# Kernel tuning notes

Hardware: AMD Instinct MI355X
Metric: run time of the kernel (lower is better)

Reference implementation:

```python
import jax, jax.numpy as jnp
import numpy as np

EPS = 1e-5

def conv1x1(x, w, b):
    # x: [B,C,H,W], w: [O,C], b: [O]
    return jnp.einsum('bchw,oc->bohw', x, w) + b[None, :, None, None]

def bn_eval(x, w, b, m, v):
    inv = w / jnp.sqrt(v + EPS)
    return (x - m[None, :, None, None]) * inv[None, :, None, None] + b[None, :, None, None]

def setup_inputs() -> dict:
    key = jax.random.key(0)
    ks = jax.random.split(key, 32)
    B, Fg, Fl, Fi, H, W = 4, 128, 128, 64, 64, 64
    d = {}
    d['g'] = jax.random.normal(ks[0], (B, Fg, H, W), jnp.float32)
    d['x'] = jax.random.normal(ks[1], (B, Fl, H, W), jnp.float32)
    d['wg_w'] = jax.random.normal(ks[2], (Fi, Fg), jnp.float32) * 0.1
    d['wg_b'] = jax.random.normal(ks[3], (Fi,), jnp.float32) * 0.1
    d['bng_w'] = jax.random.uniform(ks[4], (Fi,), jnp.float32)
    d['bng_b'] = jax.random.normal(ks[5], (Fi,), jnp.float32) * 0.1
    d['bng_m'] = jax.random.normal(ks[6], (Fi,), jnp.float32) * 0.1
    d['bng_v'] = jax.random.uniform(ks[7], (Fi,), jnp.float32) + 0.5
    d['wx_w'] = jax.random.normal(ks[8], (Fi, Fl), jnp.float32) * 0.1
    d['wx_b'] = jax.random.normal(ks[9], (Fi,), jnp.float32) * 0.1
    d['bnx_w'] = jax.random.uniform(ks[10], (Fi,), jnp.float32)
    d['bnx_b'] = jax.random.normal(ks[11], (Fi,), jnp.float32) * 0.1
    d['bnx_m'] = jax.random.normal(ks[12], (Fi,), jnp.float32) * 0.1
    d['bnx_v'] = jax.random.uniform(ks[13], (Fi,), jnp.float32) + 0.5
    d['q_w'] = jax.random.normal(ks[14], (Fi // 8, Fi), jnp.float32) * 0.1
    d['q_b'] = jax.random.normal(ks[15], (Fi // 8,), jnp.float32) * 0.1
    d['k_w'] = jax.random.normal(ks[16], (Fi // 8, Fi), jnp.float32) * 0.1
    d['k_b'] = jax.random.normal(ks[17], (Fi // 8,), jnp.float32) * 0.1
    d['v_w'] = jax.random.normal(ks[18], (Fi, Fi), jnp.float32) * 0.1
    d['v_b'] = jax.random.normal(ks[19], (Fi,), jnp.float32) * 0.1
    d['sa_gamma'] = jax.random.normal(ks[20], (1,), jnp.float32)
    d['psi_w'] = jax.random.normal(ks[21], (1, Fi), jnp.float32) * 0.1
    d['psi_b'] = jax.random.normal(ks[22], (1,), jnp.float32) * 0.1
    d['bnp_w'] = jax.random.uniform(ks[23], (1,), jnp.float32)
    d['bnp_b'] = jax.random.normal(ks[24], (1,), jnp.float32) * 0.1
    d['bnp_m'] = jax.random.normal(ks[25], (1,), jnp.float32) * 0.1
    d['bnp_v'] = jax.random.uniform(ks[26], (1,), jnp.float32) + 0.5
    return d

def reference(g, x, wg_w, wg_b, bng_w, bng_b, bng_m, bng_v,
              wx_w, wx_b, bnx_w, bnx_b, bnx_m, bnx_v,
              q_w, q_b, k_w, k_b, v_w, v_b, sa_gamma,
              psi_w, psi_b, bnp_w, bnp_b, bnp_m, bnp_v):
    g1 = bn_eval(conv1x1(g, wg_w, wg_b), bng_w, bng_b, bng_m, bng_v)
    x1 = bn_eval(conv1x1(x, wx_w, wx_b), bnx_w, bnx_b, bnx_m, bnx_v)
    c = jax.nn.relu(g1 + x1)  # [B, Fi, H, W]
    B, C, H, W = c.shape
    N = H * W
    q = conv1x1(c, q_w, q_b).reshape(B, -1, N)  # [B, Fi/8, N]
    k = conv1x1(c, k_w, k_b).reshape(B, -1, N)
    v = conv1x1(c, v_w, v_b).reshape(B, C, N)
    energy = jnp.einsum('bcn,bcm->bnm', q, k)    # [B, N, N]
    attn = jax.nn.softmax(energy, axis=-1)
    sa_out = jnp.einsum('bcm,bnm->bcn', v, attn).reshape(B, C, H, W)
    attended = sa_gamma[0] * sa_out + c
    psi = jax.nn.sigmoid(bn_eval(conv1x1(attended, psi_w, psi_b), bnp_w, bnp_b, bnp_m, bnp_v))
    return x * psi
```

## Files before the change

### kernel.cpp

```cpp
#include <hip/hip_runtime.h>
#include <hip/hip_bf16.h>


typedef short bf16x8 __attribute__((ext_vector_type(8)));
typedef unsigned short u16x8 __attribute__((ext_vector_type(8)));
typedef unsigned short u16x4 __attribute__((ext_vector_type(4)));
typedef float f32x4 __attribute__((ext_vector_type(4)));

__device__ __forceinline__ unsigned short f2b16(float f) {
  return __builtin_bit_cast(unsigned short, __float2bfloat16(f));
}
__device__ __forceinline__ float b2f(unsigned short u) {
  return __bfloat162float(__builtin_bit_cast(__hip_bfloat16, u));
}

#define EPSV 1e-5f
#define LOG2E 1.44269504088896340736f

#define C_OFF      0u
#define Q_OFF      (C_OFF + 2097152u)
#define K_OFF      (Q_OFF + 262144u)
#define V_OFF      (K_OFF + 262144u)
#define OPART_OFF  (V_OFF + 2097152u)
#define ML_OFF     (OPART_OFF + 16777216u)

__global__ __launch_bounds__(256) void conv_fused_kernel(
    const float* __restrict__ g, const float* __restrict__ x,
    const float* __restrict__ wg_w, const float* __restrict__ wg_b,
    const float* __restrict__ bng_w, const float* __restrict__ bng_b,
    const float* __restrict__ bng_m, const float* __restrict__ bng_v,
    const float* __restrict__ wx_w, const float* __restrict__ wx_b,
    const float* __restrict__ bnx_w, const float* __restrict__ bnx_b,
    const float* __restrict__ bnx_m, const float* __restrict__ bnx_v,
    const float* __restrict__ q_w, const float* __restrict__ q_b,
    const float* __restrict__ k_w, const float* __restrict__ k_b,
    const float* __restrict__ v_w, const float* __restrict__ v_b,
    unsigned short* __restrict__ cb, unsigned short* __restrict__ Qb,
    unsigned short* __restrict__ Kb, unsigned short* __restrict__ Vb)
{
  __shared__ __attribute__((aligned(16))) unsigned short xt[32][264];
  __shared__ __attribute__((aligned(16))) unsigned short clds[32][72];
  __shared__ __attribute__((aligned(16))) unsigned short vstage[64][36];

  const int t = threadIdx.x;
  const int bid = blockIdx.x;
  const int b = bid >> 7;
  const int n0 = (bid & 127) << 5;

  {
    const int col4 = t & 7;
    const int rowg = t >> 3;
    float4 v[8];
    #pragma unroll
    for (int rr = 0; rr < 8; ++rr) {
      int row = rowg * 8 + rr;
      const float* src = (row < 128)
          ? (g + ((size_t)(b * 128 + row)) * 4096 + n0 + col4 * 4)
          : (x + ((size_t)(b * 128 + (row - 128))) * 4096 + n0 + col4 * 4);
      v[rr] = *(const float4*)src;
    }
    #pragma unroll
    for (int j = 0; j < 4; ++j) {
      u16x8 pk;
      #pragma unroll
      for (int rr = 0; rr < 8; ++rr)
        pk[rr] = f2b16(((const float*)&v[rr])[j]);
      *(u16x8*)(&xt[col4 * 4 + j][rowg * 8]) = pk;
    }
  }

  const int l = t & 63, w = t >> 6;
  const int l15 = l & 15, lg = l >> 4;
  f32x4 zf = {0.f, 0.f, 0.f, 0.f};

  const int orow = w * 16 + l15;
  const float invg = bng_w[orow] * rsqrtf(bng_v[orow] + EPSV);
  const float invx = bnx_w[orow] * rsqrtf(bnx_v[orow] + EPSV);
  bf16x8 afrag[8];
  #pragma unroll
  for (int ks = 0; ks < 8; ++ks) {
    int k = ks * 32 + lg * 8;
    const float* wp;
    float sc;
    if (k < 128) { wp = wg_w + orow * 128 + k;         sc = invg; }
    else         { wp = wx_w + orow * 128 + (k - 128); sc = invx; }
    float4 w0 = *(const float4*)wp;
    float4 w1 = *(const float4*)(wp + 4);
    u16x8 pk;
    pk[0] = f2b16(w0.x * sc); pk[1] = f2b16(w0.y * sc);
    pk[2] = f2b16(w0.z * sc); pk[3] = f2b16(w0.w * sc);
    pk[4] = f2b16(w1.x * sc); pk[5] = f2b16(w1.y * sc);
    pk[6] = f2b16(w1.z * sc); pk[7] = f2b16(w1.w * sc);
    afrag[ks] = __builtin_bit_cast(bf16x8, pk);
  }
  __syncthreads();

  f32x4 acc[2];
  acc[0] = acc[1] = zf;
  #pragma unroll
  for (int ks = 0; ks < 8; ++ks) {
    #pragma unroll
    for (int ns = 0; ns < 2; ++ns) {
      bf16x8 bfv = *(const bf16x8*)(&xt[ns * 16 + l15][ks * 32 + lg * 8]);
      acc[ns] = __builtin_amdgcn_mfma_f32_16x16x32_bf16(afrag[ks], bfv, acc[ns], 0, 0, 0);
    }
  }
  #pragma unroll
  for (int r = 0; r < 4; ++r) {
    int o = w * 16 + lg * 4 + r;
    float ig = bng_w[o] * rsqrtf(bng_v[o] + EPSV);
    float ix = bnx_w[o] * rsqrtf(bnx_v[o] + EPSV);
    float bc = (wg_b[o] - bng_m[o]) * ig + bng_b[o]
             + (wx_b[o] - bnx_m[o]) * ix + bnx_b[o];
    #pragma unroll
    for (int ns = 0; ns < 2; ++ns) {
      float cv = fmaxf(acc[ns][r] + bc, 0.f);
      unsigned short cv16 = f2b16(cv);
      cb[((size_t)(b * 64 + o)) * 4096 + n0 + ns * 16 + l15] = cv16;
      clds[ns * 16 + l15][o] = cv16;
    }
  }
  __syncthreads();

  #pragma unroll
  for (int i = 0; i < 3; ++i) {
    int tau = w + 4 * i;
    if (tau >= 10) break;
    int t5 = tau % 5, ns = tau / 5;
    int wrow = t5 * 16 + l15;
    f32x4 a2 = zf;
    #pragma unroll
    for (int kk = 0; kk < 2; ++kk) {
      int k = kk * 32 + lg * 8;
      const float* wp = (wrow < 8)  ? (q_w + wrow * 64 + k)
                      : (wrow < 16) ? (k_w + (wrow - 8) * 64 + k)
                                    : (v_w + (wrow - 16) * 64 + k);
      float4 w0 = *(const float4*)wp;
      float4 w1 = *(const float4*)(wp + 4);
      u16x8 pk;
      pk[0] = f2b16(w0.x); pk[1] = f2b16(w0.y);
      pk[2] = f2b16(w0.z); pk[3] = f2b16(w0.w);
      pk[4] = f2b16(w1.x); pk[5] = f2b16(w1.y);
      pk[6] = f2b16(w1.z); pk[7] = f2b16(w1.w);
      bf16x8 bfv = *(const bf16x8*)(&clds[ns * 16 + l15][k]);
      a2 = __builtin_amdgcn_mfma_f32_16x16x32_bf16(
          __builtin_bit_cast(bf16x8, pk), bfv, a2, 0, 0, 0);
    }
    int ngl = n0 + ns * 16 + l15;
    if (t5 == 0) {
      u16x4 pk;
      #pragma unroll
      for (int r = 0; r < 4; ++r) {
        int row = lg * 4 + r;
        float val;
        if (row < 8) val = (a2[r] + q_b[row]) * LOG2E;
        else         val = a2[r] + k_b[row - 8];
        pk[r] = f2b16(val);
      }
      if (lg < 2)
        *(u16x4*)(Qb + (((size_t)b << 12) + ngl) * 8 + lg * 4) = pk;
      else
        *(u16x4*)(Kb + (((size_t)b << 12) + ngl) * 8 + (lg - 2) * 4) = pk;
    } else {
      #pragma unroll
      for (int r = 0; r < 4; ++r) {
        int vch = (t5 - 1) * 16 + lg * 4 + r;
        vstage[vch][ns * 16 + l15] = f2b16(a2[r] + v_b[vch]);
      }
    }
  }
  __syncthreads();

  #pragma unroll
  for (int i = 0; i < 2; ++i) {
    int idx = t + 256 * i;
    int row = idx >> 3, seg = idx & 7;
    u16x4 pv = *(const u16x4*)(&vstage[row][seg * 4]);
    *(u16x4*)(Vb + ((size_t)(b * 64 + row)) * 4096 + n0 + seg * 4) = pv;
  }
}

__global__ __launch_bounds__(256) void attn_partial_kernel(
    const unsigned short* __restrict__ Qb, const unsigned short* __restrict__ Kb,
    const unsigned short* __restrict__ Vb,
    unsigned short* __restrict__ Opart, float* __restrict__ ml)
{
  __shared__ __attribute__((aligned(16))) unsigned short klds[64][8];
  __shared__ __attribute__((aligned(16))) unsigned short vlds[64][72];
  __shared__ __attribute__((aligned(16))) unsigned short plds[4][2][16][40];

  const int t = threadIdx.x;
  const int bid = blockIdx.x;
  const int qt = bid & 63;
  const int b = (bid >> 6) & 3;
  const int ci = bid >> 8;
  const int n0 = qt << 6;
  const int l = t & 63, w = t >> 6;
  const int l15 = l & 15, lg = l >> 4;

  bf16x8 qf = {0, 0, 0, 0, 0, 0, 0, 0};
  if (lg == 0)
    qf = *(const bf16x8*)(Qb + (((size_t)b << 12) + n0 + w * 16 + l15) * 8);

  f32x4 zf = {0.f, 0.f, 0.f, 0.f};
  f32x4 O[4];
  O[0] = O[1] = O[2] = O[3] = zf;
  float m_run = -INFINITY;
  float l_run = 0.f;

  const int vrow0 = t >> 3, voff0 = t & 7;
  const unsigned short* Kb_base = Kb + ((size_t)b << 12) * 8;
  const unsigned short* Vb_base = Vb + ((size_t)(b * 64)) * 4096;

  const int m_lo = ci << 9, m_hi = (ci + 1) << 9;

  int4 kreg{}, vreg0{}, vreg1{};
  if (t < 64)
    kreg = *(const int4*)(Kb_base + (size_t)(m_lo + t) * 8);
  vreg0 = *(const int4*)(Vb_base + (size_t)vrow0 * 4096 + m_lo + voff0 * 8);
  vreg1 = *(const int4*)(Vb_base + (size_t)(vrow0 + 32) * 4096 + m_lo + voff0 * 8);

  for (int m0 = m_lo; m0 < m_hi; m0 += 64) {
    if (t < 64) *(int4*)(&klds[t][0]) = kreg;
    *(int4*)(&vlds[vrow0][voff0 * 8]) = vreg0;
    *(int4*)(&vlds[vrow0 + 32][voff0 * 8]) = vreg1;
    __syncthreads();

    if (m0 + 64 < m_hi) {
      if (t < 64)
        kreg = *(const int4*)(Kb_base + (size_t)(m0 + 64 + t) * 8);
      vreg0 = *(const int4*)(Vb_base + (size_t)vrow0 * 4096 + (m0 + 64) + voff0 * 8);
      vreg1 = *(const int4*)(Vb_base + (size_t)(vrow0 + 32) * 4096 + (m0 + 64) + voff0 * 8);
    }

    f32x4 e[4];
    #pragma unroll
    for (int mt = 0; mt < 4; ++mt) {
      bf16x8 kf = *(const bf16x8*)(&klds[mt * 16 + l15][0]);
      e[mt] = __builtin_amdgcn_mfma_f32_16x16x32_bf16(kf, qf, zf, 0, 0, 0);
    }

    float vm = fmaxf(fmaxf(fmaxf(e[0][0], e[0][1]), fmaxf(e[0][2], e[0][3])),
                     fmaxf(fmaxf(e[1][0], e[1][1]), fmaxf(e[1][2], e[1][3])));
    float vm2 = fmaxf(fmaxf(fmaxf(e[2][0], e[2][1]), fmaxf(e[2][2], e[2][3])),
                      fmaxf(fmaxf(e[3][0], e[3][1]), fmaxf(e[3][2], e[3][3])));
    vm = fmaxf(vm, vm2);
    vm = fmaxf(vm, __shfl_xor(vm, 16));
    vm = fmaxf(vm, __shfl_xor(vm, 32));

    bool nosk = __any(vm > m_run + 8.f);
    float nm = nosk ? fmaxf(m_run, vm) : m_run;
    float s = 0.f;
    #pragma unroll
    for (int mt = 0; mt < 4; ++mt) {
      #pragma unroll
      for (int r = 0; r < 4; ++r) {
        float p = __builtin_amdgcn_exp2f(e[mt][r] - nm);
        e[mt][r] = p;
        s += p;
      }
    }
    s += __shfl_xor(s, 16);
    s += __shfl_xor(s, 32);
    if (nosk) {
      float sc = __builtin_amdgcn_exp2f(m_run - nm);
      l_run = l_run * sc + s;
      m_run = nm;
      #pragma unroll
      for (int ct = 0; ct < 4; ++ct)
        #pragma unroll
        for (int r = 0; r < 4; ++r) O[ct][r] *= sc;
    } else {
      l_run += s;
    }

    #pragma unroll
    for (int mt = 0; mt < 4; ++mt) {
      u16x4 pk;
      #pragma unroll
      for (int r = 0; r < 4; ++r) pk[r] = f2b16(e[mt][r]);
      int kk = mt >> 1;
      int lgr = 2 * (mt & 1) + (lg >> 1);
      int j0 = 4 * (lg & 1);
      *(u16x4*)(&plds[w][kk][l15][lgr * 8 + j0]) = pk;
    }

    #pragma unroll
    for (int ct = 0; ct < 4; ++ct) {
      #pragma unroll
      for (int kk = 0; kk < 2; ++kk) {
        bf16x8 pfr = *(const bf16x8*)(&plds[w][kk][l15][lg * 8]);
        bf16x8 vf = *(const bf16x8*)(&vlds[ct * 16 + l15][kk * 32 + lg * 8]);
        O[ct] = __builtin_amdgcn_mfma_f32_16x16x32_bf16(vf, pfr, O[ct], 0, 0, 0);
      }
    }
    __syncthreads();
  }

  const size_t pb = ((size_t)(ci * 4 + b)) << 12;
  const int qg = n0 + w * 16 + l15;
  #pragma unroll
  for (int ct = 0; ct < 4; ++ct) {
    u16x4 pk;
    #pragma unroll
    for (int r = 0; r < 4; ++r) pk[r] = f2b16(O[ct][r]);
    *(u16x4*)(Opart + (pb + qg) * 64 + ct * 16 + lg * 4) = pk;
  }
  if (lg == 0) {
    float2 mv;
    mv.x = m_run; mv.y = l_run;
    *(float2*)(ml + (pb + qg) * 2) = mv;
  }
}

__global__ __launch_bounds__(256) void combine_kernel(
    const unsigned short* __restrict__ Opart, const float* __restrict__ ml,
    const unsigned short* __restrict__ cb, const float* __restrict__ xin,
    const float* __restrict__ psi_w, const float* __restrict__ psi_b,
    const float* __restrict__ bnp_w, const float* __restrict__ bnp_b,
    const float* __restrict__ bnp_m, const float* __restrict__ bnp_v,
    const float* __restrict__ sa_gamma,
    float* __restrict__ out)
{
  __shared__ __attribute__((aligned(16))) unsigned short c_lds[64][20];
  __shared__ __attribute__((aligned(8))) float2 ml_lds[16][8];
  __shared__ float psi_lds[16];

  const int t = threadIdx.x;
  const int bid = blockIdx.x;
  const int b = bid >> 8;
  const int n0 = (bid & 255) << 4;

  {
    int row = t >> 2, seg = t & 3;
    *(u16x4*)(&c_lds[row][seg * 4]) =
        *(const u16x4*)(cb + ((size_t)(b * 64 + row)) * 4096 + n0 + seg * 4);
  }
  if (t < 128) {
    int q = t >> 3, ci = t & 7;
    ml_lds[q][ci] = *(const float2*)(ml + ((((size_t)(ci * 4 + b)) << 12) + n0 + q) * 2);
  }
  __syncthreads();

  const float invp = bnp_w[0] * rsqrtf(bnp_v[0] + EPSV);
  const float psi_c = (psi_b[0] - bnp_m[0]) * invp + bnp_b[0];
  const float gamma = sa_gamma[0];

  const int q = t >> 4, cg = t & 15;
  const int qg = n0 + q;

  float M = -INFINITY;
  #pragma unroll
  for (int ci = 0; ci < 8; ++ci) M = fmaxf(M, ml_lds[q][ci].x);
  float L = 0.f, wgt[8];
  #pragma unroll
  for (int ci = 0; ci < 8; ++ci) {
    wgt[ci] = __builtin_amdgcn_exp2f(ml_lds[q][ci].x - M);
    L += wgt[ci] * ml_lds[q][ci].y;
  }
  float o4[4] = {0.f, 0.f, 0.f, 0.f};
  #pragma unroll
  for (int ci = 0; ci < 8; ++ci) {
    u16x4 p = *(const u16x4*)(Opart + ((((size_t)(ci * 4 + b)) << 12) + qg) * 64 + cg * 4);
    float wv = wgt[ci];
    #pragma unroll
    for (int k = 0; k < 4; ++k) o4[k] += wv * b2f(p[k]);
  }
  const float invL = 1.f / L;
  float ps = 0.f;
  #pragma unroll
  for (int k = 0; k < 4; ++k) {
    int ch = cg * 4 + k;
    ps += (psi_w[ch] * invp) * (gamma * (o4[k] * invL) + b2f(c_lds[ch][q]));
  }
  ps += __shfl_xor(ps, 1);
  ps += __shfl_xor(ps, 2);
  ps += __shfl_xor(ps, 4);
  ps += __shfl_xor(ps, 8);
  if (cg == 0)
    psi_lds[q] = 1.f / (1.f + __expf(-(ps + psi_c)));
  __syncthreads();

  #pragma unroll
  for (int i = 0; i < 2; ++i) {
    int idx = t + 256 * i;
    int f = idx >> 2, c4 = idx & 3;
    size_t off = ((size_t)(b * 128 + f)) * 4096 + n0 + c4 * 4;
    float4 xv = *(const float4*)(xin + off);
    float4 ov;
    ov.x = xv.x * psi_lds[c4 * 4 + 0];
    ov.y = xv.y * psi_lds[c4 * 4 + 1];
    ov.z = xv.z * psi_lds[c4 * 4 + 2];
    ov.w = xv.w * psi_lds[c4 * 4 + 3];
    *(float4*)(out + off) = ov;
  }
}

extern "C" void kernel_launch(void* const* d_in, const int* in_sizes, int n_in,
                              void* d_out, int out_size, void* d_ws, size_t ws_size,
                              hipStream_t stream) {
  (void)in_sizes; (void)n_in; (void)out_size; (void)ws_size;
  const float* g     = (const float*)d_in[0];
  const float* x     = (const float*)d_in[1];
  const float* wg_w  = (const float*)d_in[2];
  const float* wg_b  = (const float*)d_in[3];
  const float* bng_w = (const float*)d_in[4];
  const float* bng_b = (const float*)d_in[5];
  const float* bng_m = (const float*)d_in[6];
  const float* bng_v = (const float*)d_in[7];
  const float* wx_w  = (const float*)d_in[8];
  const float* wx_b  = (const float*)d_in[9];
  const float* bnx_w = (const float*)d_in[10];
  const float* bnx_b = (const float*)d_in[11];
  const float* bnx_m = (const float*)d_in[12];
  const float* bnx_v = (const float*)d_in[13];
  const float* q_w   = (const float*)d_in[14];
  const float* q_b   = (const float*)d_in[15];
  const float* k_w   = (const float*)d_in[16];
  const float* k_b   = (const float*)d_in[17];
  const float* v_w   = (const float*)d_in[18];
  const float* v_b   = (const float*)d_in[19];
  const float* sa_g  = (const float*)d_in[20];
  const float* psi_w = (const float*)d_in[21];
  const float* psi_b = (const float*)d_in[22];
  const float* bnp_w = (const float*)d_in[23];
  const float* bnp_b = (const float*)d_in[24];
  const float* bnp_m = (const float*)d_in[25];
  const float* bnp_v = (const float*)d_in[26];
  float* out = (float*)d_out;

  char* ws = (char*)d_ws;
  unsigned short* cb = (unsigned short*)(ws + C_OFF);
  unsigned short* Qb = (unsigned short*)(ws + Q_OFF);
  unsigned short* Kb = (unsigned short*)(ws + K_OFF);
  unsigned short* Vb = (unsigned short*)(ws + V_OFF);
  unsigned short* Opart = (unsigned short*)(ws + OPART_OFF);
  float* mlb = (float*)(ws + ML_OFF);

  hipLaunchKernelGGL(conv_fused_kernel, dim3(512), dim3(256), 0, stream,
                     g, x, wg_w, wg_b, bng_w, bng_b, bng_m, bng_v,
                     wx_w, wx_b, bnx_w, bnx_b, bnx_m, bnx_v,
                     q_w, q_b, k_w, k_b, v_w, v_b,
                     cb, Qb, Kb, Vb);

  hipLaunchKernelGGL(attn_partial_kernel, dim3(2048), dim3(256), 0, stream,
                     Qb, Kb, Vb, Opart, mlb);

  hipLaunchKernelGGL(combine_kernel, dim3(1024), dim3(256), 0, stream,
                     Opart, mlb, cb, x,
                     psi_w, psi_b, bnp_w, bnp_b, bnp_m, bnp_v, sa_g,
                     out);
}
```

Before: 160.4 us.

## Process two query tiles per attention block to reuse staged K/V tiles

Each attention-partial block now handles 128 queries (two 64-query subtiles) instead of 64, so every K/V tile staged into shared memory feeds twice the MFMA work. The grid is halved to 1024 blocks. This cuts global K/V traffic and per-tile staging and barrier overhead per query. In exchange it raises register pressure (two O accumulators and two running max/sum pairs) and halves the block count, which may hurt occupancy or tail balance on the GPU.

```diff
diff --git a/kernel.cpp b/kernel.cpp
--- a/kernel.cpp
+++ b/kernel.cpp
@@ -191,22 +191,27 @@
 
   const int t = threadIdx.x;
   const int bid = blockIdx.x;
-  const int qt = bid & 63;
-  const int b = (bid >> 6) & 3;
-  const int ci = bid >> 8;
-  const int n0 = qt << 6;
+  const int qp = bid & 31;
+  const int b = (bid >> 5) & 3;
+  const int ci = bid >> 7;
+  const int n0 = qp << 7;
   const int l = t & 63, w = t >> 6;
   const int l15 = l & 15, lg = l >> 4;
 
-  bf16x8 qf = {0, 0, 0, 0, 0, 0, 0, 0};
-  if (lg == 0)
-    qf = *(const bf16x8*)(Qb + (((size_t)b << 12) + n0 + w * 16 + l15) * 8);
+  bf16x8 qf0 = {0, 0, 0, 0, 0, 0, 0, 0};
+  bf16x8 qf1 = {0, 0, 0, 0, 0, 0, 0, 0};
+  if (lg == 0) {
+    qf0 = *(const bf16x8*)(Qb + (((size_t)b << 12) + n0 + w * 16 + l15) * 8);
+    qf1 = *(const bf16x8*)(Qb + (((size_t)b << 12) + n0 + 64 + w * 16 + l15) * 8);
+  }
 
   f32x4 zf = {0.f, 0.f, 0.f, 0.f};
-  f32x4 O[4];
-  O[0] = O[1] = O[2] = O[3] = zf;
-  float m_run = -INFINITY;
-  float l_run = 0.f;
+  f32x4 O[2][4];
+  #pragma unroll
+  for (int qt = 0; qt < 2; ++qt)
+    O[qt][0] = O[qt][1] = O[qt][2] = O[qt][3] = zf;
+  float m_run[2] = {-INFINITY, -INFINITY};
+  float l_run[2] = {0.f, 0.f};
 
   const int vrow0 = t >> 3, voff0 = t & 7;
   const unsigned short* Kb_base = Kb + ((size_t)b << 12) * 8;
@@ -233,83 +238,91 @@
       vreg1 = *(const int4*)(Vb_base + (size_t)(vrow0 + 32) * 4096 + (m0 + 64) + voff0 * 8);
     }
 
-    f32x4 e[4];
-    #pragma unroll
-    for (int mt = 0; mt < 4; ++mt) {
-      bf16x8 kf = *(const bf16x8*)(&klds[mt * 16 + l15][0]);
-      e[mt] = __builtin_amdgcn_mfma_f32_16x16x32_bf16(kf, qf, zf, 0, 0, 0);
-    }
-
-    float vm = fmaxf(fmaxf(fmaxf(e[0][0], e[0][1]), fmaxf(e[0][2], e[0][3])),
-                     fmaxf(fmaxf(e[1][0], e[1][1]), fmaxf(e[1][2], e[1][3])));
-    float vm2 = fmaxf(fmaxf(fmaxf(e[2][0], e[2][1]), fmaxf(e[2][2], e[2][3])),
-                      fmaxf(fmaxf(e[3][0], e[3][1]), fmaxf(e[3][2], e[3][3])));
-    vm = fmaxf(vm, vm2);
-    vm = fmaxf(vm, __shfl_xor(vm, 16));
-    vm = fmaxf(vm, __shfl_xor(vm, 32));
-
-    bool nosk = __any(vm > m_run + 8.f);
-    float nm = nosk ? fmaxf(m_run, vm) : m_run;
-    float s = 0.f;
-    #pragma unroll
-    for (int mt = 0; mt < 4; ++mt) {
-      #pragma unroll
-      for (int r = 0; r < 4; ++r) {
-        float p = __builtin_amdgcn_exp2f(e[mt][r] - nm);
-        e[mt][r] = p;
-        s += p;
-      }
-    }
-    s += __shfl_xor(s, 16);
-    s += __shfl_xor(s, 32);
-    if (nosk) {
-      float sc = __builtin_amdgcn_exp2f(m_run - nm);
-      l_run = l_run * sc + s;
-      m_run = nm;
-      #pragma unroll
-      for (int ct = 0; ct < 4; ++ct)
+    #pragma unroll
+    for (int qt = 0; qt < 2; ++qt) {
+      bf16x8 qf = qt ? qf1 : qf0;
+
+      f32x4 e[4];
+      #pragma unroll
+      for (int mt = 0; mt < 4; ++mt) {
+        bf16x8 kf = *(const bf16x8*)(&klds[mt * 16 + l15][0]);
+        e[mt] = __builtin_amdgcn_mfma_f32_16x16x32_bf16(kf, qf, zf, 0, 0, 0);
+      }
+
+      float vm = fmaxf(fmaxf(fmaxf(e[0][0], e[0][1]), fmaxf(e[0][2], e[0][3])),
+                       fmaxf(fmaxf(e[1][0], e[1][1]), fmaxf(e[1][2], e[1][3])));
+      float vm2 = fmaxf(fmaxf(fmaxf(e[2][0], e[2][1]), fmaxf(e[2][2], e[2][3])),
+                        fmaxf(fmaxf(e[3][0], e[3][1]), fmaxf(e[3][2], e[3][3])));
+      vm = fmaxf(vm, vm2);
+      vm = fmaxf(vm, __shfl_xor(vm, 16));
+      vm = fmaxf(vm, __shfl_xor(vm, 32));
+
+      bool nosk = __any(vm > m_run[qt] + 8.f);
+      float nm = nosk ? fmaxf(m_run[qt], vm) : m_run[qt];
+      float s = 0.f;
+      #pragma unroll
+      for (int mt = 0; mt < 4; ++mt) {
         #pragma unroll
-        for (int r = 0; r < 4; ++r) O[ct][r] *= sc;
-    } else {
-      l_run += s;
-    }
-
-    #pragma unroll
-    for (int mt = 0; mt < 4; ++mt) {
+        for (int r = 0; r < 4; ++r) {
+          float p = __builtin_amdgcn_exp2f(e[mt][r] - nm);
+          e[mt][r] = p;
+          s += p;
+        }
+      }
+      s += __shfl_xor(s, 16);
+      s += __shfl_xor(s, 32);
+      if (nosk) {
+        float sc = __builtin_amdgcn_exp2f(m_run[qt] - nm);
+        l_run[qt] = l_run[qt] * sc + s;
+        m_run[qt] = nm;
+        #pragma unroll
+        for (int ct = 0; ct < 4; ++ct)
+          #pragma unroll
+          for (int r = 0; r < 4; ++r) O[qt][ct][r] *= sc;
+      } else {
+        l_run[qt] += s;
+      }
+
+      #pragma unroll
+      for (int mt = 0; mt < 4; ++mt) {
+        u16x4 pk;
+        #pragma unroll
+        for (int r = 0; r < 4; ++r) pk[r] = f2b16(e[mt][r]);
+        int kk = mt >> 1;
+        int lgr = 2 * (mt & 1) + (lg >> 1);
+        int j0 = 4 * (lg & 1);
+        *(u16x4*)(&plds[w][kk][l15][lgr * 8 + j0]) = pk;
+      }
+
+      #pragma unroll
+      for (int ct = 0; ct < 4; ++ct) {
+        #pragma unroll
+        for (int kk = 0; kk < 2; ++kk) {
+          bf16x8 pfr = *(const bf16x8*)(&plds[w][kk][l15][lg * 8]);
+          bf16x8 vf = *(const bf16x8*)(&vlds[ct * 16 + l15][kk * 32 + lg * 8]);
+          O[qt][ct] = __builtin_amdgcn_mfma_f32_16x16x32_bf16(vf, pfr, O[qt][ct], 0, 0, 0);
+        }
+      }
+    }
+    __syncthreads();
+  }
+
+  const size_t pb = ((size_t)(ci * 4 + b)) << 12;
+  #pragma unroll
+  for (int qt = 0; qt < 2; ++qt) {
+    const int qg = n0 + qt * 64 + w * 16 + l15;
+    #pragma unroll
+    for (int ct = 0; ct < 4; ++ct) {
       u16x4 pk;
       #pragma unroll
-      for (int r = 0; r < 4; ++r) pk[r] = f2b16(e[mt][r]);
-      int kk = mt >> 1;
-      int lgr = 2 * (mt & 1) + (lg >> 1);
-      int j0 = 4 * (lg & 1);
-      *(u16x4*)(&plds[w][kk][l15][lgr * 8 + j0]) = pk;
-    }
-
-    #pragma unroll
-    for (int ct = 0; ct < 4; ++ct) {
-      #pragma unroll
-      for (int kk = 0; kk < 2; ++kk) {
-        bf16x8 pfr = *(const bf16x8*)(&plds[w][kk][l15][lg * 8]);
-        bf16x8 vf = *(const bf16x8*)(&vlds[ct * 16 + l15][kk * 32 + lg * 8]);
-        O[ct] = __builtin_amdgcn_mfma_f32_16x16x32_bf16(vf, pfr, O[ct], 0, 0, 0);
-      }
-    }
-    __syncthreads();
-  }
-
-  const size_t pb = ((size_t)(ci * 4 + b)) << 12;
-  const int qg = n0 + w * 16 + l15;
-  #pragma unroll
-  for (int ct = 0; ct < 4; ++ct) {
-    u16x4 pk;
-    #pragma unroll
-    for (int r = 0; r < 4; ++r) pk[r] = f2b16(O[ct][r]);
-    *(u16x4*)(Opart + (pb + qg) * 64 + ct * 16 + lg * 4) = pk;
-  }
-  if (lg == 0) {
-    float2 mv;
-    mv.x = m_run; mv.y = l_run;
-    *(float2*)(ml + (pb + qg) * 2) = mv;
+      for (int r = 0; r < 4; ++r) pk[r] = f2b16(O[qt][ct][r]);
+      *(u16x4*)(Opart + (pb + qg) * 64 + ct * 16 + lg * 4) = pk;
+    }
+    if (lg == 0) {
+      float2 mv;
+      mv.x = m_run[qt]; mv.y = l_run[qt];
+      *(float2*)(ml + (pb + qg) * 2) = mv;
+    }
   }
 }
 
@@ -443,7 +456,7 @@
                      q_w, q_b, k_w, k_b, v_w, v_b,
                      cb, Qb, Kb, Vb);
 
-  hipLaunchKernelGGL(attn_partial_kernel, dim3(2048), dim3(256), 0, stream,
+  hipLaunchKernelGGL(attn_partial_kernel, dim3(1024), dim3(256), 0, stream,
                      Qb, Kb, Vb, Opart, mlb);
 
   hipLaunchKernelGGL(combine_kernel, dim3(1024), dim3(256), 0, stream,
```

After: 165.3 us. 3.0% more time.
